# Kernel optimization log

Hardware: AMD Instinct MI355X
Metric: run time of the kernel (lower is better)

Reference implementation:

```python
import jax, jax.numpy as jnp
import numpy as np

N, E, IN, HID, OUT, B = 50000, 800000, 128, 128, 64, 4096
EPS = 1e-5


def setup_inputs() -> dict:
    key = jax.random.key(0)
    ks = jax.random.split(key, 12)
    x = jax.random.normal(ks[0], (N, IN), jnp.float32)
    edge_index = jax.random.randint(ks[1], (2, E), 0, N, dtype=jnp.int32).astype(jnp.int64)
    target_index = jax.random.randint(ks[2], (B,), 0, N, dtype=jnp.int32).astype(jnp.int64)

    def lin(k, i, o):
        return jax.random.normal(k, (i, o), jnp.float32) * (1.0 / np.sqrt(i))

    return {
        'x': x, 'edge_index': edge_index, 'target_index': target_index,
        'W0': lin(ks[3], IN, HID), 'b0': jnp.zeros((HID,), jnp.float32),
        'W1': lin(ks[4], HID, HID), 'b1': jnp.zeros((HID,), jnp.float32),
        'W2': lin(ks[5], HID, HID), 'b2': jnp.zeros((HID,), jnp.float32),
        'g0': jnp.ones((HID,), jnp.float32), 'bt0': jnp.zeros((HID,), jnp.float32),
        'g1': jnp.ones((HID,), jnp.float32), 'bt1': jnp.zeros((HID,), jnp.float32),
        'f1w': lin(ks[6], HID, HID), 'f1b': jnp.zeros((HID,), jnp.float32),
        'f2w': lin(ks[7], HID, OUT), 'f2b': jnp.zeros((OUT,), jnp.float32),
    }


def _gcn_layer(h, W, b, src, dst, norm):
    # GCNConv: D^-1/2 (A+I) D^-1/2 (h W) + b  (self-loops already in src/dst)
    h = h @ W                                        # [N, out]
    msg = h[src] * norm[:, None]                     # [E+N, out]
    return jax.ops.segment_sum(msg, dst, num_segments=N) + b


def _batchnorm(h, g, bt):
    mu = jnp.mean(h, axis=0)
    var = jnp.mean((h - mu) ** 2, axis=0)            # biased, as torch BN
    return g * (h - mu) * jax.lax.rsqrt(var + EPS) + bt


def reference(x, edge_index, target_index, W0, b0, W1, b1, W2, b2,
              g0, bt0, g1, bt1, f1w, f1b, f2w, f2b):
    loop = jnp.arange(N, dtype=edge_index.dtype)
    src = jnp.concatenate([edge_index[0], loop])
    dst = jnp.concatenate([edge_index[1], loop])
    deg = jax.ops.segment_sum(jnp.ones_like(dst, jnp.float32), dst, num_segments=N)
    dinv = jax.lax.rsqrt(deg)                        # deg >= 1 via self-loops
    norm = dinv[src] * dinv[dst]                     # [E+N]

    h = _gcn_layer(x, W0, b0, src, dst, norm)
    h = jax.nn.relu(_batchnorm(h, g0, bt0))
    h = _gcn_layer(h, W1, b1, src, dst, norm)
    h = jax.nn.relu(_batchnorm(h, g1, bt1))
    h = _gcn_layer(h, W2, b2, src, dst, norm)

    # target_index.unsqueeze(1).expand(-1,-1) -> [B,1]; pool squeezes dim 1
    t = h[target_index]                              # [B, HID]
    t = jax.nn.relu(t @ f1w + f1b)                   # FeedForwardNetwork layer1 (dropout=0)
    return t @ f2w + f2b                             # [B, OUT]
```

## Files before the change

kernel.cpp:

```cpp
#include <hip/hip_runtime.h>


static const int GNN5566_NN  = 50000;
static const int GNN5566_NE  = 800000;
static const int GNN5566_NB  = 4096;
static const int GNN5566_CAP = 64;

static const int GNN5566_NBUCK  = (GNN5566_NN + 63) / 64;
static const int GNN5566_NCHUNK = 128;
static const int GNN5566_CHUNK  = GNN5566_NE / GNN5566_NCHUNK;

static const int GNN5566_WSLOT = 17408;

typedef short gnn5566_s16x8 __attribute__((ext_vector_type(8)));
typedef float gnn5566_f32x4 __attribute__((ext_vector_type(4)));

static __device__ inline float gnn5566_b2f(unsigned short h){
  return __uint_as_float(((unsigned int)h) << 16);
}
static __device__ inline unsigned short gnn5566_f2b(float f){
  unsigned int u = __float_as_uint(f);
  u += 0x7fffu + ((u >> 16) & 1u);
  return (unsigned short)(u >> 16);
}
static __device__ inline float gnn5566_loadf(const void* p, long long i, int isF32){
  if (isF32) return ((const float*)p)[i];
  return gnn5566_b2f(((const unsigned short*)p)[i]);
}

__global__ void GNNEncoder_5566277616090_sortA(const void* W0, const void* W1,
                                               const void* W2, const void* f1w,
                                               const void* f2w, unsigned short* wT,
                                               const int* ei, const int* tgt,
                                               int* flags, int* done,
                                               unsigned int* histC, unsigned int* prefC,
                                               unsigned int* sorted){
  __shared__ unsigned short lt[128][129];
  __shared__ int h[GNN5566_NBUCK];
  __shared__ int sv[256];
  __shared__ int sFlag;
  int b = blockIdx.x, tid = threadIdx.x;

  if (b == 133) {
    if (tid < 8) done[tid] = 0;
    if (tid < 64) {
      int o1 = ei[2*tid + 1];
      int o2 = tgt[2*tid + 1];
      unsigned int w = ((const unsigned int*)W0)[tid];
      unsigned int e = (w >> 7) & 255u;
      unsigned long long m1 = __ballot(o1 != 0);
      unsigned long long m2 = __ballot(o2 != 0);
      unsigned long long m3 = __ballot(e >= 96u && e <= 134u);
      if (tid == 0) {
        flags[0] = (m1 == 0ull) ? 1 : 0;
        flags[1] = (m2 == 0ull) ? 1 : 0;
        flags[2] = (__popcll(m3) >= 56) ? 0 : 1;
      }
    }
    return;
  }

  if (b >= 128) {
    if (tid < 64) {
      unsigned int w = ((const unsigned int*)W0)[tid];
      unsigned int e = (w >> 7) & 255u;
      unsigned long long m3 = __ballot(e >= 96u && e <= 134u);
      if (tid == 0) sFlag = (__popcll(m3) >= 56) ? 0 : 1;
    }
    __syncthreads();
    int f32 = sFlag;
    int slot = b - 128;
    const void* src = (slot == 0) ? W0 : (slot == 1) ? W1 : (slot == 2) ? W2
                    : (slot == 3) ? f1w : f2w;
    int wide = (slot != 4);
    int tot = wide ? 16384 : 8192;
    for (int i = tid; i < tot; i += 256) {
      int k = wide ? (i >> 7) : (i >> 6);
      int c = wide ? (i & 127) : (i & 63);
      lt[k][c] = f32 ? gnn5566_f2b(((const float*)src)[i])
                     : ((const unsigned short*)src)[i];
    }
    __syncthreads();
    unsigned short* out = wT + slot * GNN5566_WSLOT;
    int wtot = wide ? 2048 : 1024;
    for (int j = tid; j < wtot; j += 256) {
      int c = j >> 4, k8 = (j & 15) << 3;
      unsigned int p0 = (unsigned int)lt[k8    ][c] | ((unsigned int)lt[k8+1][c] << 16);
      unsigned int p1 = (unsigned int)lt[k8 + 2][c] | ((unsigned int)lt[k8+3][c] << 16);
      unsigned int p2 = (unsigned int)lt[k8 + 4][c] | ((unsigned int)lt[k8+5][c] << 16);
      unsigned int p3 = (unsigned int)lt[k8 + 6][c] | ((unsigned int)lt[k8+7][c] << 16);
      uint4 v; v.x = p0; v.y = p1; v.z = p2; v.w = p3;
      *(uint4*)(out + c * 136 + k8) = v;
    }
    return;
  }

  if (tid < 64) {
    int o1 = ei[2*tid + 1];
    unsigned long long m1 = __ballot(o1 != 0);
    if (tid == 0) sFlag = (m1 == 0ull) ? 1 : 0;
  }
  for (int i = tid; i < GNN5566_NBUCK; i += 256) h[i] = 0;
  __syncthreads();
  int f = sFlag;
  int base = b * GNN5566_CHUNK;

  for (int i = tid; i < GNN5566_CHUNK; i += 256) {
    int d = f ? ((const int2*)ei)[GNN5566_NE + base + i].x : ei[GNN5566_NE + base + i];
    atomicAdd(&h[d >> 6], 1);
  }
  __syncthreads();

  int b0 = tid * 4;
  int c0 = (b0     < GNN5566_NBUCK) ? h[b0]     : 0;
  int c1 = (b0 + 1 < GNN5566_NBUCK) ? h[b0 + 1] : 0;
  int c2 = (b0 + 2 < GNN5566_NBUCK) ? h[b0 + 2] : 0;
  int c3 = (b0 + 3 < GNN5566_NBUCK) ? h[b0 + 3] : 0;
  int T = c0 + c1 + c2 + c3;
  sv[tid] = T;
  __syncthreads();
  for (int off = 1; off < 256; off <<= 1) {
    int add = (tid >= off) ? sv[tid - off] : 0;
    __syncthreads();
    sv[tid] += add;
    __syncthreads();
  }
  int excl = sv[tid] - T;

  unsigned int* hrow = histC + (long long)b * GNN5566_NBUCK;
  unsigned int* prow = prefC + (long long)b * GNN5566_NBUCK;
  if (b0     < GNN5566_NBUCK) { hrow[b0]     = (unsigned int)c0;
                                prow[b0]     = (unsigned int)excl;
                                h[b0]     = excl; }
  if (b0 + 1 < GNN5566_NBUCK) { hrow[b0 + 1] = (unsigned int)c1;
                                prow[b0 + 1] = (unsigned int)(excl + c0);
                                h[b0 + 1] = excl + c0; }
  if (b0 + 2 < GNN5566_NBUCK) { hrow[b0 + 2] = (unsigned int)c2;
                                prow[b0 + 2] = (unsigned int)(excl + c0 + c1);
                                h[b0 + 2] = excl + c0 + c1; }
  if (b0 + 3 < GNN5566_NBUCK) { hrow[b0 + 3] = (unsigned int)c3;
                                prow[b0 + 3] = (unsigned int)(excl + c0 + c1 + c2);
                                h[b0 + 3] = excl + c0 + c1 + c2; }
  __syncthreads();

  for (int i = tid; i < GNN5566_CHUNK; i += 256) {
    int s, d;
    if (f) { s = ((const int2*)ei)[base + i].x;
             d = ((const int2*)ei)[GNN5566_NE + base + i].x; }
    else   { s = ei[base + i];
             d = ei[GNN5566_NE + base + i]; }
    int p = atomicAdd(&h[d >> 6], 1);
    sorted[base + p] = ((unsigned int)s << 6) | (unsigned int)(d & 63);
  }
}

__global__ void GNNEncoder_5566277616090_fillB2(const unsigned int* histC,
                                                const unsigned int* prefC,
                                                const unsigned int* sorted,
                                                unsigned short* colIdx16, int* cnt,
                                                float* dinv){
  __shared__ unsigned int lbuf[64 * 32];
  __shared__ int lcnt[64];
  int b   = blockIdx.x;
  int tid = threadIdx.x;
  if (tid < 64) lcnt[tid] = 0;
  __syncthreads();

  unsigned short* lists = (unsigned short*)lbuf;
  if (tid < GNN5566_NCHUNK) {
    int c     = tid;
    int len   = (int)histC[(long long)c * GNN5566_NBUCK + b];
    int start = c * GNN5566_CHUNK + (int)prefC[(long long)c * GNN5566_NBUCK + b];
    for (int j = 0; j < len; ++j) {
      unsigned int w = sorted[start + j];
      int d = (int)(w & 63u);
      int p = atomicAdd(&lcnt[d], 1);
      if (p < GNN5566_CAP) lists[d * 64 + p] = (unsigned short)(w >> 6);
    }
  }
  __syncthreads();

  if (tid < 64) {
    int node = b * 64 + tid;
    if (node < GNN5566_NN) {
      int c = lcnt[tid];
      cnt[node]  = c;
      dinv[node] = rsqrtf((float)(c + 1));
    }
  }
  unsigned int* out = (unsigned int*)colIdx16;
  for (int idx = tid; idx < 2048; idx += 256) {
    int d = idx >> 5;
    int node = b * 64 + d;
    if (node < GNN5566_NN)
      out[(long long)node * 32 + (idx & 31)] = lbuf[idx];
  }
}

__global__ void GNNEncoder_5566277616090_kernel(const void* A,
                                                const unsigned short* wT,
                                                unsigned short* Out, int nRows,
                                                const float* bnA, const float* bnC,
                                                const float* rowScale,
                                                const void* bias, int reluOut,
                                                int aExternal, const int* flags)
{
  __shared__ __align__(16) unsigned short gnnLw[128 * 136];
  __shared__ float lbnA[128], lbnC[128], lbias[128];
  int tid = threadIdx.x;
  int wF32 = flags[2];
  int aF32 = aExternal ? wF32 : 0;

  int wave = tid >> 6, lane = tid & 63;
  int q = lane >> 4, ln = lane & 15;
  int rowBase = blockIdx.x * 64 + wave * 16;
  int r  = rowBase + ln;
  int cr = (r < nRows) ? r : (nRows - 1);
  float rs = rowScale ? rowScale[cr] : 1.0f;
  int useBN = (bnA != 0);

  uint4  rawU[4];
  float4 rawF[8];
  if (aF32) {
    const float4* ap = (const float4*)A + (long long)cr * 32 + q * 2;
    #pragma unroll
    for (int kk = 0; kk < 4; ++kk) { rawF[2*kk] = ap[kk*8]; rawF[2*kk+1] = ap[kk*8+1]; }
  } else {
    const uint4* ap = (const uint4*)A + (long long)cr * 16 + q;
    #pragma unroll
    for (int kk = 0; kk < 4; ++kk) rawU[kk] = ap[kk * 4];
  }

  {
    const uint4* src = (const uint4*)wT;
    uint4* dst = (uint4*)gnnLw;
    for (int i = tid; i < 2176; i += 256) dst[i] = src[i];
  }
  if (tid < 128) {
    lbnA[tid]  = bnA  ? bnA[tid] : 0.0f;
    lbnC[tid]  = bnC  ? bnC[tid] : 0.0f;
    lbias[tid] = bias ? gnn5566_loadf(bias, tid, wF32) : 0.0f;
  }
  __syncthreads();

  gnn5566_s16x8 afr[4];
  #pragma unroll
  for (int kk = 0; kk < 4; ++kk) {
    int kb = kk * 32 + q * 8;
    float vals[8];
    if (aF32) {
      float4 u = rawF[2*kk], w = rawF[2*kk+1];
      vals[0] = u.x; vals[1] = u.y; vals[2] = u.z; vals[3] = u.w;
      vals[4] = w.x; vals[5] = w.y; vals[6] = w.z; vals[7] = w.w;
    } else {
      uint4 u = rawU[kk];
      vals[0] = gnn5566_b2f((unsigned short)(u.x & 0xffffu));
      vals[1] = gnn5566_b2f((unsigned short)(u.x >> 16));
      vals[2] = gnn5566_b2f((unsigned short)(u.y & 0xffffu));
      vals[3] = gnn5566_b2f((unsigned short)(u.y >> 16));
      vals[4] = gnn5566_b2f((unsigned short)(u.z & 0xffffu));
      vals[5] = gnn5566_b2f((unsigned short)(u.z >> 16));
      vals[6] = gnn5566_b2f((unsigned short)(u.w & 0xffffu));
      vals[7] = gnn5566_b2f((unsigned short)(u.w >> 16));
    }
    if (useBN) {
      float4 a0 = *(const float4*)&lbnA[kb], a1 = *(const float4*)&lbnA[kb + 4];
      float4 c0 = *(const float4*)&lbnC[kb], c1 = *(const float4*)&lbnC[kb + 4];
      vals[0] = fmaxf(vals[0] * a0.x + c0.x, 0.0f);
      vals[1] = fmaxf(vals[1] * a0.y + c0.y, 0.0f);
      vals[2] = fmaxf(vals[2] * a0.z + c0.z, 0.0f);
      vals[3] = fmaxf(vals[3] * a0.w + c0.w, 0.0f);
      vals[4] = fmaxf(vals[4] * a1.x + c1.x, 0.0f);
      vals[5] = fmaxf(vals[5] * a1.y + c1.y, 0.0f);
      vals[6] = fmaxf(vals[6] * a1.z + c1.z, 0.0f);
      vals[7] = fmaxf(vals[7] * a1.w + c1.w, 0.0f);
    }
    #pragma unroll
    for (int j = 0; j < 8; ++j) afr[kk][j] = (short)gnn5566_f2b(vals[j] * rs);
  }

  gnn5566_f32x4 zero4;
  zero4[0] = 0.0f; zero4[1] = 0.0f; zero4[2] = 0.0f; zero4[3] = 0.0f;
  gnn5566_f32x4 acc[8];
  #pragma unroll
  for (int t = 0; t < 8; ++t) acc[t] = zero4;

  #pragma unroll
  for (int kk = 0; kk < 4; ++kk) {
    int kb = kk * 32 + q * 8;
    #pragma unroll
    for (int t = 0; t < 8; ++t) {
      gnn5566_s16x8 bfr = *(const gnn5566_s16x8*)(&gnnLw[(t * 16 + ln) * 136 + kb]);
      acc[t] = __builtin_amdgcn_mfma_f32_16x16x32_bf16(afr[kk], bfr, acc[t], 0, 0, 0);
    }
  }

  __syncthreads();
  #pragma unroll
  for (int t = 0; t < 8; ++t) {
    int col = t * 16 + ln;
    float badd = lbias[col];
    #pragma unroll
    for (int rg = 0; rg < 4; ++rg) {
      float v = acc[t][rg] + badd;
      if (reluOut) v = fmaxf(v, 0.0f);
      gnnLw[(wave * 16 + q * 4 + rg) * 136 + col] = gnn5566_f2b(v);
    }
  }
  __syncthreads();
  int tRowBase = blockIdx.x * 64;
  for (int j = tid; j < 1024; j += 256) {
    int rr = j >> 4, c4 = j & 15;
    int grow = tRowBase + rr;
    if (grow < nRows) {
      uint4 v = *(const uint4*)&gnnLw[rr * 136 + c4 * 8];
      *(uint4*)&Out[(long long)grow * 128 + c4 * 8] = v;
    }
  }
}

__global__ void GNNEncoder_5566277616090_ffn(const unsigned short* A,
                                             const unsigned short* wT3,
                                             const unsigned short* wT4,
                                             void* Out, const int* tgt,
                                             const int* tgtFlag,
                                             const void* f1b, const void* fb2,
                                             const int* flags)
{
  __shared__ __align__(16) unsigned short lwA[128 * 136];
  __shared__ __align__(16) unsigned short lwB[64 * 136];
  __shared__ __align__(16) unsigned short ep[64 * 136];
  __shared__ float lb1[128];
  __shared__ float lb2[64];
  int tid = threadIdx.x;
  int f32 = flags[2];

  {
    const uint4* sA = (const uint4*)wT3;
    uint4* dA = (uint4*)lwA;
    for (int i = tid; i < 2176; i += 256) dA[i] = sA[i];
    const uint4* sB = (const uint4*)wT4;
    uint4* dB = (uint4*)lwB;
    for (int i = tid; i < 1088; i += 256) dB[i] = sB[i];
  }
  if (tid < 128) lb1[tid] = gnn5566_loadf(f1b, tid, f32);
  if (tid < 64)  lb2[tid] = gnn5566_loadf(fb2, tid, f32);
  __syncthreads();

  int wave = tid >> 6, lane = tid & 63;
  int q = lane >> 4, ln = lane & 15;
  int rowBase = blockIdx.x * 64 + wave * 16;
  int r  = rowBase + ln;
  int cr = (r < GNN5566_NB) ? r : (GNN5566_NB - 1);
  int ar = (*tgtFlag) ? tgt[2 * cr] : tgt[cr];

  gnn5566_s16x8 afr[4];
  #pragma unroll
  for (int kk = 0; kk < 4; ++kk) {
    int kb = kk * 32 + q * 8;
    const uint4* ap = (const uint4*)A + (long long)ar * 16 + (kb >> 3);
    uint4 u = ap[0];
    unsigned short e[8];
    e[0] = (unsigned short)(u.x & 0xffffu); e[1] = (unsigned short)(u.x >> 16);
    e[2] = (unsigned short)(u.y & 0xffffu); e[3] = (unsigned short)(u.y >> 16);
    e[4] = (unsigned short)(u.z & 0xffffu); e[5] = (unsigned short)(u.z >> 16);
    e[6] = (unsigned short)(u.w & 0xffffu); e[7] = (unsigned short)(u.w >> 16);
    #pragma unroll
    for (int j = 0; j < 8; ++j) afr[kk][j] = (short)e[j];
  }

  gnn5566_f32x4 zero4;
  zero4[0] = 0.0f; zero4[1] = 0.0f; zero4[2] = 0.0f; zero4[3] = 0.0f;
  gnn5566_f32x4 acc[8];
  #pragma unroll
  for (int t = 0; t < 8; ++t) acc[t] = zero4;
  #pragma unroll
  for (int kk = 0; kk < 4; ++kk) {
    int kb = kk * 32 + q * 8;
    #pragma unroll
    for (int t = 0; t < 8; ++t) {
      gnn5566_s16x8 bfr = *(const gnn5566_s16x8*)(&lwA[(t * 16 + ln) * 136 + kb]);
      acc[t] = __builtin_amdgcn_mfma_f32_16x16x32_bf16(afr[kk], bfr, acc[t], 0, 0, 0);
    }
  }
  #pragma unroll
  for (int t = 0; t < 8; ++t) {
    int col = t * 16 + ln;
    float badd = lb1[col];
    #pragma unroll
    for (int rg = 0; rg < 4; ++rg) {
      float v = fmaxf(acc[t][rg] + badd, 0.0f);
      ep[(wave * 16 + q * 4 + rg) * 136 + col] = gnn5566_f2b(v);
    }
  }
  __syncthreads();

  gnn5566_s16x8 afr2[4];
  #pragma unroll
  for (int kk = 0; kk < 4; ++kk) {
    int kb = kk * 32 + q * 8;
    afr2[kk] = *(const gnn5566_s16x8*)(&ep[(wave * 16 + ln) * 136 + kb]);
  }
  gnn5566_f32x4 acc2[4];
  #pragma unroll
  for (int t = 0; t < 4; ++t) acc2[t] = zero4;
  #pragma unroll
  for (int kk = 0; kk < 4; ++kk) {
    int kb = kk * 32 + q * 8;
    #pragma unroll
    for (int t = 0; t < 4; ++t) {
      gnn5566_s16x8 bfr = *(const gnn5566_s16x8*)(&lwB[(t * 16 + ln) * 136 + kb]);
      acc2[t] = __builtin_amdgcn_mfma_f32_16x16x32_bf16(afr2[kk], bfr, acc2[t], 0, 0, 0);
    }
  }
  #pragma unroll
  for (int t = 0; t < 4; ++t) {
    int col = t * 16 + ln;
    float badd = lb2[col];
    #pragma unroll
    for (int rg = 0; rg < 4; ++rg) {
      int grow = rowBase + q * 4 + rg;
      if (grow < GNN5566_NB) {
        float v = acc2[t][rg] + badd;
        if (f32) ((float*)Out)[(long long)grow * 64 + col] = v;
        else     ((unsigned short*)Out)[(long long)grow * 64 + col] = gnn5566_f2b(v);
      }
    }
  }
}

__global__ void GNNEncoder_5566277616090_agg(const unsigned short* hs,
                                             const unsigned short* colIdx16,
                                             const int* cnt, const float* dinv,
                                             const void* bias, unsigned short* ha,
                                             const int* flags)
{
  int gw = (int)((blockIdx.x * 256u + threadIdx.x) >> 6);
  if (gw >= GNN5566_NN) return;
  int lane = threadIdx.x & 63;
  const unsigned int* hrow = (const unsigned int*)hs;
  unsigned int sv = hrow[(long long)gw * 64 + lane];
  float a0 = __uint_as_float(sv << 16);
  float a1 = __uint_as_float(sv & 0xffff0000u);
  int m = cnt[gw]; if (m > GNN5566_CAP) m = GNN5566_CAP;
  const unsigned short* cp = colIdx16 + (long long)gw * GNN5566_CAP;
  const uint4* cp4 = (const uint4*)cp;
  int i = 0;
  for (; i + 16 <= m; i += 16) {
    uint4 iwA = cp4[i >> 3];
    uint4 iwB = cp4[(i >> 3) + 1];
    unsigned int v0  = hrow[(long long)(iwA.x & 0xffffu) * 64 + lane];
    unsigned int v1  = hrow[(long long)(iwA.x >> 16)     * 64 + lane];
    unsigned int v2  = hrow[(long long)(iwA.y & 0xffffu) * 64 + lane];
    unsigned int v3  = hrow[(long long)(iwA.y >> 16)     * 64 + lane];
    unsigned int v4  = hrow[(long long)(iwA.z & 0xffffu) * 64 + lane];
    unsigned int v5  = hrow[(long long)(iwA.z >> 16)     * 64 + lane];
    unsigned int v6  = hrow[(long long)(iwA.w & 0xffffu) * 64 + lane];
    unsigned int v7  = hrow[(long long)(iwA.w >> 16)     * 64 + lane];
    unsigned int v8  = hrow[(long long)(iwB.x & 0xffffu) * 64 + lane];
    unsigned int v9  = hrow[(long long)(iwB.x >> 16)     * 64 + lane];
    unsigned int v10 = hrow[(long long)(iwB.y & 0xffffu) * 64 + lane];
    unsigned int v11 = hrow[(long long)(iwB.y >> 16)     * 64 + lane];
    unsigned int v12 = hrow[(long long)(iwB.z & 0xffffu) * 64 + lane];
    unsigned int v13 = hrow[(long long)(iwB.z >> 16)     * 64 + lane];
    unsigned int v14 = hrow[(long long)(iwB.w & 0xffffu) * 64 + lane];
    unsigned int v15 = hrow[(long long)(iwB.w >> 16)     * 64 + lane];
    a0 += __uint_as_float(v0  << 16) + __uint_as_float(v1  << 16)
        + __uint_as_float(v2  << 16) + __uint_as_float(v3  << 16)
        + __uint_as_float(v4  << 16) + __uint_as_float(v5  << 16)
        + __uint_as_float(v6  << 16) + __uint_as_float(v7  << 16)
        + __uint_as_float(v8  << 16) + __uint_as_float(v9  << 16)
        + __uint_as_float(v10 << 16) + __uint_as_float(v11 << 16)
        + __uint_as_float(v12 << 16) + __uint_as_float(v13 << 16)
        + __uint_as_float(v14 << 16) + __uint_as_float(v15 << 16);
    a1 += __uint_as_float(v0  & 0xffff0000u) + __uint_as_float(v1  & 0xffff0000u)
        + __uint_as_float(v2  & 0xffff0000u) + __uint_as_float(v3  & 0xffff0000u)
        + __uint_as_float(v4  & 0xffff0000u) + __uint_as_float(v5  & 0xffff0000u)
        + __uint_as_float(v6  & 0xffff0000u) + __uint_as_float(v7  & 0xffff0000u)
        + __uint_as_float(v8  & 0xffff0000u) + __uint_as_float(v9  & 0xffff0000u)
        + __uint_as_float(v10 & 0xffff0000u) + __uint_as_float(v11 & 0xffff0000u)
        + __uint_as_float(v12 & 0xffff0000u) + __uint_as_float(v13 & 0xffff0000u)
        + __uint_as_float(v14 & 0xffff0000u) + __uint_as_float(v15 & 0xffff0000u);
  }
  for (; i + 8 <= m; i += 8) {
    uint4 iw = cp4[i >> 3];
    unsigned int v0 = hrow[(long long)(iw.x & 0xffffu) * 64 + lane];
    unsigned int v1 = hrow[(long long)(iw.x >> 16)     * 64 + lane];
    unsigned int v2 = hrow[(long long)(iw.y & 0xffffu) * 64 + lane];
    unsigned int v3 = hrow[(long long)(iw.y >> 16)     * 64 + lane];
    unsigned int v4 = hrow[(long long)(iw.z & 0xffffu) * 64 + lane];
    unsigned int v5 = hrow[(long long)(iw.z >> 16)     * 64 + lane];
    unsigned int v6 = hrow[(long long)(iw.w & 0xffffu) * 64 + lane];
    unsigned int v7 = hrow[(long long)(iw.w >> 16)     * 64 + lane];
    a0 += __uint_as_float(v0 << 16) + __uint_as_float(v1 << 16)
        + __uint_as_float(v2 << 16) + __uint_as_float(v3 << 16)
        + __uint_as_float(v4 << 16) + __uint_as_float(v5 << 16)
        + __uint_as_float(v6 << 16) + __uint_as_float(v7 << 16);
    a1 += __uint_as_float(v0 & 0xffff0000u) + __uint_as_float(v1 & 0xffff0000u)
        + __uint_as_float(v2 & 0xffff0000u) + __uint_as_float(v3 & 0xffff0000u)
        + __uint_as_float(v4 & 0xffff0000u) + __uint_as_float(v5 & 0xffff0000u)
        + __uint_as_float(v6 & 0xffff0000u) + __uint_as_float(v7 & 0xffff0000u);
  }
  for (; i < m; ++i) {
    unsigned int v = hrow[(long long)cp[i] * 64 + lane];
    a0 += __uint_as_float(v << 16);
    a1 += __uint_as_float(v & 0xffff0000u);
  }
  float s = dinv[gw];
  int f32 = flags[2];
  float o0 = a0 * s + gnn5566_loadf(bias, lane * 2,     f32);
  float o1 = a1 * s + gnn5566_loadf(bias, lane * 2 + 1, f32);
  unsigned int packed = (unsigned int)gnn5566_f2b(o0)
                      | (((unsigned int)gnn5566_f2b(o1)) << 16);
  ((unsigned int*)ha)[(long long)gw * 64 + lane] = packed;
}

__global__ void GNNEncoder_5566277616090_stats(const unsigned short* ha, float* partial,
                                               const void* g, const void* bt,
                                               float* bnA, float* bnC,
                                               const int* flags, int* doneCtr){
  __shared__ float red[256];
  __shared__ int lastFlag;
  const unsigned int* h32 = (const unsigned int*)ha;
  int tid = threadIdx.x;
  int cp2 = tid & 63, sub = tid >> 6;
  float s0 = 0.0f, s1 = 0.0f, q0 = 0.0f, q1 = 0.0f;
  for (int r = blockIdx.x * 4 + sub; r < GNN5566_NN; r += 512) {
    unsigned int v = h32[(long long)r * 64 + cp2];
    float a = __uint_as_float(v << 16);
    float b = __uint_as_float(v & 0xffff0000u);
    s0 += a; q0 += a * a; s1 += b; q1 += b * b;
  }
  float* prow = partial + blockIdx.x * 256;
  red[tid] = s0; __syncthreads();
  if (sub == 0) atomicExch(&prow[2*cp2],
      red[cp2] + red[64+cp2] + red[128+cp2] + red[192+cp2]);
  __syncthreads();
  red[tid] = s1; __syncthreads();
  if (sub == 0) atomicExch(&prow[2*cp2 + 1],
      red[cp2] + red[64+cp2] + red[128+cp2] + red[192+cp2]);
  __syncthreads();
  red[tid] = q0; __syncthreads();
  if (sub == 0) atomicExch(&prow[128 + 2*cp2],
      red[cp2] + red[64+cp2] + red[128+cp2] + red[192+cp2]);
  __syncthreads();
  red[tid] = q1; __syncthreads();
  if (sub == 0) atomicExch(&prow[128 + 2*cp2 + 1],
      red[cp2] + red[64+cp2] + red[128+cp2] + red[192+cp2]);
  __syncthreads();

  if (tid == 0) {
    __threadfence();
    lastFlag = (atomicAdd(doneCtr, 1) == (int)gridDim.x - 1);
  }
  __syncthreads();
  if (!lastFlag) return;

  float acc = 0.0f;
  for (int b = 0; b < (int)gridDim.x; b += 8) {
    float p0 = atomicAdd(&partial[(b    ) * 256 + tid], 0.0f);
    float p1 = atomicAdd(&partial[(b + 1) * 256 + tid], 0.0f);
    float p2 = atomicAdd(&partial[(b + 2) * 256 + tid], 0.0f);
    float p3 = atomicAdd(&partial[(b + 3) * 256 + tid], 0.0f);
    float p4 = atomicAdd(&partial[(b + 4) * 256 + tid], 0.0f);
    float p5 = atomicAdd(&partial[(b + 5) * 256 + tid], 0.0f);
    float p6 = atomicAdd(&partial[(b + 6) * 256 + tid], 0.0f);
    float p7 = atomicAdd(&partial[(b + 7) * 256 + tid], 0.0f);
    acc += ((p0 + p1) + (p2 + p3)) + ((p4 + p5) + (p6 + p7));
  }
  red[tid] = acc;
  __syncthreads();
  if (tid < 128) {
    int f32 = flags[2];
    float invN = 1.0f / (float)GNN5566_NN;
    float mu  = red[tid] * invN;
    float var = red[128 + tid] * invN - mu * mu;
    if (var < 0.0f) var = 0.0f;
    float a = gnn5566_loadf(g, tid, f32) * rsqrtf(var + 1e-5f);
    bnA[tid] = a;
    bnC[tid] = gnn5566_loadf(bt, tid, f32) - mu * a;
  }
}

extern "C" void kernel_launch(void* const* d_in, const int* in_sizes, int n_in,
                              void* d_out, int out_size, void* d_ws, size_t ws_size,
                              hipStream_t stream)
{
  const void* x   = d_in[0];
  const int*  ei  = (const int*)d_in[1];
  const int*  tgt = (const int*)d_in[2];
  const void* W0  = d_in[3];
  const void* b0  = d_in[4];
  const void* W1  = d_in[5];
  const void* b1  = d_in[6];
  const void* W2  = d_in[7];
  const void* b2  = d_in[8];
  const void* g0  = d_in[9];
  const void* bt0 = d_in[10];
  const void* g1  = d_in[11];
  const void* bt1 = d_in[12];
  const void* f1w = d_in[13];
  const void* f1b = d_in[14];
  const void* f2w = d_in[15];
  const void* fb2 = d_in[16];

  char* ws = (char*)d_ws;
  int*            cnt      = (int*)           (ws + 8192);
  float*          dinv     = (float*)         (ws + 208896);
  unsigned short* wT       = (unsigned short*)(ws + 409600);
  unsigned int*   histC    = (unsigned int*)  (ws + 583936);
  unsigned int*   prefC    = (unsigned int*)  (ws + 984320);
  unsigned int*   sorted   = (unsigned int*)  (ws + 1384960);
  unsigned short* colIdx16 = (unsigned short*)(ws + 4585216);
  unsigned short* hs       = (unsigned short*)(ws + 10985472);
  unsigned short* ha       = (unsigned short*)(ws + 23785728);
  float*          partial  = (float*)         (ws + 36585984);
  float*          bn       = (float*)         (ws + 36848128);
  int*            flags    = (int*)           (ws + 36850176);
  int*            done     = (int*)           (ws + 36850432);

  float* bn0A = bn;       float* bn0C = bn + 128;
  float* bn1A = bn + 256; float* bn1C = bn + 384;

  GNNEncoder_5566277616090_sortA <<<134, 256, 0, stream>>>(
      W0, W1, W2, f1w, f2w, wT, ei, tgt, flags, done, histC, prefC, sorted);
  GNNEncoder_5566277616090_fillB2<<<GNN5566_NBUCK, 256, 0, stream>>>(
      histC, prefC, sorted, colIdx16, cnt, dinv);

  const int gemmGrid = (GNN5566_NN + 63) / 64;

  GNNEncoder_5566277616090_kernel<<<gemmGrid, 256, 0, stream>>>(
      x, wT, hs, GNN5566_NN, (const float*)0, (const float*)0, dinv,
      (const void*)0, 0, 1, flags);
  GNNEncoder_5566277616090_agg  <<<12500, 256, 0, stream>>>(hs, colIdx16, cnt, dinv, b0, ha, flags);
  GNNEncoder_5566277616090_stats<<<128, 256, 0, stream>>>(
      ha, partial, g0, bt0, bn0A, bn0C, flags, done + 1);

  GNNEncoder_5566277616090_kernel<<<gemmGrid, 256, 0, stream>>>(
      ha, wT + GNN5566_WSLOT, hs, GNN5566_NN, bn0A, bn0C, dinv,
      (const void*)0, 0, 0, flags);
  GNNEncoder_5566277616090_agg  <<<12500, 256, 0, stream>>>(hs, colIdx16, cnt, dinv, b1, ha, flags);
  GNNEncoder_5566277616090_stats<<<128, 256, 0, stream>>>(
      ha, partial + 32768, g1, bt1, bn1A, bn1C, flags, done + 2);

  GNNEncoder_5566277616090_kernel<<<gemmGrid, 256, 0, stream>>>(
      ha, wT + 2 * GNN5566_WSLOT, hs, GNN5566_NN, bn1A, bn1C, dinv,
      (const void*)0, 0, 0, flags);
  GNNEncoder_5566277616090_agg  <<<12500, 256, 0, stream>>>(hs, colIdx16, cnt, dinv, b2, ha, flags);

  GNNEncoder_5566277616090_ffn<<<64, 256, 0, stream>>>(
      ha, wT + 3 * GNN5566_WSLOT, wT + 4 * GNN5566_WSLOT, d_out,
      tgt, flags + 1, f1b, fb2, flags);
}
```

Before: 356.7 us.

## Split aggregation row across four blocks with neighbor-parallel sub-waves

The aggregation kernel is restructured so that each node's 64 packed columns are split into four 16-column quarters, each handled by a different block. Within a wave, four 16-lane groups process different neighbors concurrently and combine their partial sums with cross-lane shuffles. The grid grows from 12500 to 50000 blocks. The intent is more parallelism per node and shorter dependent loops for the short neighbor lists (average about 16). The cost is 64-byte rather than 256-byte gathers, three-quarters of lanes idle on the store, extra shuffle work and more blocks to launch.

```diff
diff --git a/kernel.cpp b/kernel.cpp
--- a/kernel.cpp
+++ b/kernel.cpp
@@ -435,84 +435,60 @@
                                              const void* bias, unsigned short* ha,
                                              const int* flags)
 {
-  int gw = (int)((blockIdx.x * 256u + threadIdx.x) >> 6);
+  int wave = threadIdx.x >> 6;
+  int q    = blockIdx.x & 3;
+  int gw   = ((blockIdx.x >> 2) << 2) + wave;
   if (gw >= GNN5566_NN) return;
   int lane = threadIdx.x & 63;
+  int sub  = lane >> 4;
+  int c    = lane & 15;
+  int colU = q * 16 + c;
   const unsigned int* hrow = (const unsigned int*)hs;
-  unsigned int sv = hrow[(long long)gw * 64 + lane];
-  float a0 = __uint_as_float(sv << 16);
-  float a1 = __uint_as_float(sv & 0xffff0000u);
+
+  float a0 = 0.0f, a1 = 0.0f;
   int m = cnt[gw]; if (m > GNN5566_CAP) m = GNN5566_CAP;
   const unsigned short* cp = colIdx16 + (long long)gw * GNN5566_CAP;
-  const uint4* cp4 = (const uint4*)cp;
   int i = 0;
   for (; i + 16 <= m; i += 16) {
-    uint4 iwA = cp4[i >> 3];
-    uint4 iwB = cp4[(i >> 3) + 1];
-    unsigned int v0  = hrow[(long long)(iwA.x & 0xffffu) * 64 + lane];
-    unsigned int v1  = hrow[(long long)(iwA.x >> 16)     * 64 + lane];
-    unsigned int v2  = hrow[(long long)(iwA.y & 0xffffu) * 64 + lane];
-    unsigned int v3  = hrow[(long long)(iwA.y >> 16)     * 64 + lane];
-    unsigned int v4  = hrow[(long long)(iwA.z & 0xffffu) * 64 + lane];
-    unsigned int v5  = hrow[(long long)(iwA.z >> 16)     * 64 + lane];
-    unsigned int v6  = hrow[(long long)(iwA.w & 0xffffu) * 64 + lane];
-    unsigned int v7  = hrow[(long long)(iwA.w >> 16)     * 64 + lane];
-    unsigned int v8  = hrow[(long long)(iwB.x & 0xffffu) * 64 + lane];
-    unsigned int v9  = hrow[(long long)(iwB.x >> 16)     * 64 + lane];
-    unsigned int v10 = hrow[(long long)(iwB.y & 0xffffu) * 64 + lane];
-    unsigned int v11 = hrow[(long long)(iwB.y >> 16)     * 64 + lane];
-    unsigned int v12 = hrow[(long long)(iwB.z & 0xffffu) * 64 + lane];
-    unsigned int v13 = hrow[(long long)(iwB.z >> 16)     * 64 + lane];
-    unsigned int v14 = hrow[(long long)(iwB.w & 0xffffu) * 64 + lane];
-    unsigned int v15 = hrow[(long long)(iwB.w >> 16)     * 64 + lane];
-    a0 += __uint_as_float(v0  << 16) + __uint_as_float(v1  << 16)
-        + __uint_as_float(v2  << 16) + __uint_as_float(v3  << 16)
-        + __uint_as_float(v4  << 16) + __uint_as_float(v5  << 16)
-        + __uint_as_float(v6  << 16) + __uint_as_float(v7  << 16)
-        + __uint_as_float(v8  << 16) + __uint_as_float(v9  << 16)
-        + __uint_as_float(v10 << 16) + __uint_as_float(v11 << 16)
-        + __uint_as_float(v12 << 16) + __uint_as_float(v13 << 16)
-        + __uint_as_float(v14 << 16) + __uint_as_float(v15 << 16);
-    a1 += __uint_as_float(v0  & 0xffff0000u) + __uint_as_float(v1  & 0xffff0000u)
-        + __uint_as_float(v2  & 0xffff0000u) + __uint_as_float(v3  & 0xffff0000u)
-        + __uint_as_float(v4  & 0xffff0000u) + __uint_as_float(v5  & 0xffff0000u)
-        + __uint_as_float(v6  & 0xffff0000u) + __uint_as_float(v7  & 0xffff0000u)
-        + __uint_as_float(v8  & 0xffff0000u) + __uint_as_float(v9  & 0xffff0000u)
-        + __uint_as_float(v10 & 0xffff0000u) + __uint_as_float(v11 & 0xffff0000u)
-        + __uint_as_float(v12 & 0xffff0000u) + __uint_as_float(v13 & 0xffff0000u)
-        + __uint_as_float(v14 & 0xffff0000u) + __uint_as_float(v15 & 0xffff0000u);
-  }
-  for (; i + 8 <= m; i += 8) {
-    uint4 iw = cp4[i >> 3];
-    unsigned int v0 = hrow[(long long)(iw.x & 0xffffu) * 64 + lane];
-    unsigned int v1 = hrow[(long long)(iw.x >> 16)     * 64 + lane];
-    unsigned int v2 = hrow[(long long)(iw.y & 0xffffu) * 64 + lane];
-    unsigned int v3 = hrow[(long long)(iw.y >> 16)     * 64 + lane];
-    unsigned int v4 = hrow[(long long)(iw.z & 0xffffu) * 64 + lane];
-    unsigned int v5 = hrow[(long long)(iw.z >> 16)     * 64 + lane];
-    unsigned int v6 = hrow[(long long)(iw.w & 0xffffu) * 64 + lane];
-    unsigned int v7 = hrow[(long long)(iw.w >> 16)     * 64 + lane];
+    int i0 = cp[i + sub], i1 = cp[i + 4 + sub];
+    int i2 = cp[i + 8 + sub], i3 = cp[i + 12 + sub];
+    unsigned int v0 = hrow[(long long)i0 * 64 + colU];
+    unsigned int v1 = hrow[(long long)i1 * 64 + colU];
+    unsigned int v2 = hrow[(long long)i2 * 64 + colU];
+    unsigned int v3 = hrow[(long long)i3 * 64 + colU];
     a0 += __uint_as_float(v0 << 16) + __uint_as_float(v1 << 16)
-        + __uint_as_float(v2 << 16) + __uint_as_float(v3 << 16)
-        + __uint_as_float(v4 << 16) + __uint_as_float(v5 << 16)
-        + __uint_as_float(v6 << 16) + __uint_as_float(v7 << 16);
+        + __uint_as_float(v2 << 16) + __uint_as_float(v3 << 16);
     a1 += __uint_as_float(v0 & 0xffff0000u) + __uint_as_float(v1 & 0xffff0000u)
-        + __uint_as_float(v2 & 0xffff0000u) + __uint_as_float(v3 & 0xffff0000u)
-        + __uint_as_float(v4 & 0xffff0000u) + __uint_as_float(v5 & 0xffff0000u)
-        + __uint_as_float(v6 & 0xffff0000u) + __uint_as_float(v7 & 0xffff0000u);
-  }
-  for (; i < m; ++i) {
-    unsigned int v = hrow[(long long)cp[i] * 64 + lane];
+        + __uint_as_float(v2 & 0xffff0000u) + __uint_as_float(v3 & 0xffff0000u);
+  }
+  for (; i + 4 <= m; i += 4) {
+    int ix = cp[i + sub];
+    unsigned int v = hrow[(long long)ix * 64 + colU];
     a0 += __uint_as_float(v << 16);
     a1 += __uint_as_float(v & 0xffff0000u);
   }
+  if (i + sub < m) {
+    int ix = cp[i + sub];
+    unsigned int v = hrow[(long long)ix * 64 + colU];
+    a0 += __uint_as_float(v << 16);
+    a1 += __uint_as_float(v & 0xffff0000u);
+  }
+
+  a0 += __shfl_xor(a0, 16, 64); a0 += __shfl_xor(a0, 32, 64);
+  a1 += __shfl_xor(a1, 16, 64); a1 += __shfl_xor(a1, 32, 64);
+
+  unsigned int sv = hrow[(long long)gw * 64 + colU];
   float s = dinv[gw];
   int f32 = flags[2];
-  float o0 = a0 * s + gnn5566_loadf(bias, lane * 2,     f32);
-  float o1 = a1 * s + gnn5566_loadf(bias, lane * 2 + 1, f32);
-  unsigned int packed = (unsigned int)gnn5566_f2b(o0)
-                      | (((unsigned int)gnn5566_f2b(o1)) << 16);
-  ((unsigned int*)ha)[(long long)gw * 64 + lane] = packed;
+  float o0 = (a0 + __uint_as_float(sv << 16)) * s
+           + gnn5566_loadf(bias, colU * 2,     f32);
+  float o1 = (a1 + __uint_as_float(sv & 0xffff0000u)) * s
+           + gnn5566_loadf(bias, colU * 2 + 1, f32);
+  if (sub == 0) {
+    unsigned int packed = (unsigned int)gnn5566_f2b(o0)
+                        | (((unsigned int)gnn5566_f2b(o1)) << 16);
+    ((unsigned int*)ha)[(long long)gw * 64 + colU] = packed;
+  }
 }
 
 __global__ void GNNEncoder_5566277616090_stats(const unsigned short* ha, float* partial,
@@ -628,25 +604,26 @@
       histC, prefC, sorted, colIdx16, cnt, dinv);
 
   const int gemmGrid = (GNN5566_NN + 63) / 64;
+  const int aggGrid  = 50000;
 
   GNNEncoder_5566277616090_kernel<<<gemmGrid, 256, 0, stream>>>(
       x, wT, hs, GNN5566_NN, (const float*)0, (const float*)0, dinv,
       (const void*)0, 0, 1, flags);
-  GNNEncoder_5566277616090_agg  <<<12500, 256, 0, stream>>>(hs, colIdx16, cnt, dinv, b0, ha, flags);
+  GNNEncoder_5566277616090_agg  <<<aggGrid, 256, 0, stream>>>(hs, colIdx16, cnt, dinv, b0, ha, flags);
   GNNEncoder_5566277616090_stats<<<128, 256, 0, stream>>>(
       ha, partial, g0, bt0, bn0A, bn0C, flags, done + 1);
 
   GNNEncoder_5566277616090_kernel<<<gemmGrid, 256, 0, stream>>>(
       ha, wT + GNN5566_WSLOT, hs, GNN5566_NN, bn0A, bn0C, dinv,
       (const void*)0, 0, 0, flags);
-  GNNEncoder_5566277616090_agg  <<<12500, 256, 0, stream>>>(hs, colIdx16, cnt, dinv, b1, ha, flags);
+  GNNEncoder_5566277616090_agg  <<<aggGrid, 256, 0, stream>>>(hs, colIdx16, cnt, dinv, b1, ha, flags);
   GNNEncoder_5566277616090_stats<<<128, 256, 0, stream>>>(
       ha, partial + 32768, g1, bt1, bn1A, bn1C, flags, done + 2);
 
   GNNEncoder_5566277616090_kernel<<<gemmGrid, 256, 0, stream>>>(
       ha, wT + 2 * GNN5566_WSLOT, hs, GNN5566_NN, bn1A, bn1C, dinv,
       (const void*)0, 0, 0, flags);
-  GNNEncoder_5566277616090_agg  <<<12500, 256, 0, stream>>>(hs, colIdx16, cnt, dinv, b2, ha, flags);
+  GNNEncoder_5566277616090_agg  <<<aggGrid, 256, 0, stream>>>(hs, colIdx16, cnt, dinv, b2, ha, flags);
 
   GNNEncoder_5566277616090_ffn<<<64, 256, 0, stream>>>(
       ha, wT + 3 * GNN5566_WSLOT, wT + 4 * GNN5566_WSLOT, d_out,
```

Measured after the change: 493.3 us. 1.38x slower.
